# Optimization experiments

Measured on AMD Instinct MI355X. Metric: run time of the kernel, lower is better.

Reference implementation:

```python
import jax, jax.numpy as jnp
import numpy as np

N_NODES = 100000


def leaky(x):
    return jax.nn.leaky_relu(x, negative_slope=0.01)


def gcn_conv(h, W, b, src, dst, n_nodes):
    """PyG GCNConv: add self-loops, symmetric deg^{-1/2} normalization, scatter-add."""
    h = h @ W  # [N, out]
    deg = jax.ops.segment_sum(jnp.ones_like(dst, dtype=h.dtype), dst, num_segments=n_nodes) + 1.0  # +1 self-loop
    dinv = jax.lax.rsqrt(deg)  # deg >= 1 always
    norm = dinv[src] * dinv[dst]  # [E]
    msg = h[src] * norm[:, None]  # gather + scale, [E, out]
    agg = jax.ops.segment_sum(msg, dst, num_segments=n_nodes)
    agg = agg + h * (dinv * dinv)[:, None]  # self-loop message
    return agg + b


def setup_inputs() -> dict:
    key = jax.random.key(0)
    ks = jax.random.split(key, 16)
    num_teams = 100000
    n_edges = 5000000
    n_matches = 1000000
    x = jax.random.randint(ks[0], (N_NODES, 1), 0, num_teams)
    edge_index = jax.random.randint(ks[1], (2, n_edges), 0, N_NODES)
    home = jax.random.randint(ks[2], (n_matches,), 0, N_NODES)
    away = jax.random.randint(ks[3], (n_matches,), 0, N_NODES)
    emb = jax.random.normal(ks[4], (num_teams, 3), dtype=jnp.float32)
    W1 = jax.random.normal(ks[5], (3, 16), dtype=jnp.float32) * (1.0 / np.sqrt(3))
    b1 = jnp.zeros((16,), dtype=jnp.float32)
    W2 = jax.random.normal(ks[6], (16, 3), dtype=jnp.float32) * 0.25
    b2 = jnp.zeros((3,), dtype=jnp.float32)
    lw1 = jax.random.normal(ks[7], (6, 16), dtype=jnp.float32) * (1.0 / np.sqrt(6))
    lb1 = jnp.zeros((16,), dtype=jnp.float32)
    lw2 = jax.random.normal(ks[8], (16, 6), dtype=jnp.float32) * 0.25
    lb2 = jnp.zeros((6,), dtype=jnp.float32)
    lw3 = jax.random.normal(ks[9], (6, 3), dtype=jnp.float32) * (1.0 / np.sqrt(6))
    lb3 = jnp.zeros((3,), dtype=jnp.float32)
    return dict(x=x, edge_index=edge_index, home=home, away=away, emb=emb,
                W1=W1, b1=b1, W2=W2, b2=b2,
                lw1=lw1, lb1=lb1, lw2=lw2, lb2=lb2, lw3=lw3, lb3=lb3)


def reference(x, edge_index, home, away, emb, W1, b1, W2, b2, lw1, lb1, lw2, lb2, lw3, lb3):
    src, dst = edge_index[0], edge_index[1]
    h = emb[x[:, 0]]  # embedding lookup + squeeze(1) -> [N, 3]
    h = leaky(gcn_conv(h, W1, b1, src, dst, N_NODES))  # [N, 16]
    h = leaky(gcn_conv(h, W2, b2, src, dst, N_NODES))  # [N, 3]
    z = jnp.concatenate([h[home], h[away]], axis=-1)  # [M, 6]
    z = leaky(z @ lw1 + lb1)
    z = leaky(z @ lw2 + lb2)
    z = leaky(z @ lw3 + lb3)
    return z.reshape(-1, 3)
```

## Files before the change

### kernel.cpp

```cpp
#include <hip/hip_runtime.h>

typedef unsigned int u32;
typedef unsigned short u16;

static __device__ __forceinline__ float leaky(float v) {
    return v >= 0.0f ? v : 0.01f * v;
}

#define P1_CHUNK 8192
#define P1_T 256
#define NBK 512
#define P2_T 256
#define ASPLIT 4
#define SBLK 1024
#define S1F 8388608.0f
#define S2F 2097152.0f

static __device__ __forceinline__ int ghat(const int* __restrict__ gh,
                                           const int* __restrict__ bsum,
                                           int i, int ghN, int nE) {
    return (i == ghN) ? nE : gh[i] + bsum[i >> 10];
}

__global__ void k_p1hist(const int* __restrict__ dst, int* __restrict__ gh,
                         int nE, int nb) {
    __shared__ int hist[NBK];
    int t = threadIdx.x;
    hist[t] = 0; hist[t + 256] = 0;
    __syncthreads();
    int base = blockIdx.x * P1_CHUNK;
    int lim = min(P1_CHUNK, nE - base);
    if (lim == P1_CHUNK) {
        const int4* p = (const int4*)(dst + base);
        for (int i = t; i < P1_CHUNK / 4; i += P1_T) {
            int4 v = p[i];
            atomicAdd(&hist[v.x >> 8], 1);
            atomicAdd(&hist[v.y >> 8], 1);
            atomicAdd(&hist[v.z >> 8], 1);
            atomicAdd(&hist[v.w >> 8], 1);
        }
    } else {
        for (int i = t; i < lim; i += P1_T)
            atomicAdd(&hist[dst[base + i] >> 8], 1);
    }
    __syncthreads();
    gh[t * nb + blockIdx.x] = hist[t];
    gh[(t + 256) * nb + blockIdx.x] = hist[t + 256];
}

__global__ void g_scanA(const int* __restrict__ in, int* __restrict__ out,
                        int* __restrict__ bsum, int n) {
    __shared__ int s[SBLK];
    int t = threadIdx.x, i = blockIdx.x * SBLK + t;
    int v = (i < n) ? in[i] : 0;
    s[t] = v;
    for (int o = 1; o < SBLK; o <<= 1) {
        __syncthreads();
        int x = (t >= o) ? s[t - o] : 0;
        __syncthreads();
        s[t] += x;
    }
    __syncthreads();
    if (i < n) out[i] = s[t] - v;
    if (t == SBLK - 1) bsum[blockIdx.x] = s[t];
}
__global__ void g_scanB(int* __restrict__ bsum, int nb) {
    __shared__ int s[SBLK];
    int t = threadIdx.x;
    int v = (t < nb) ? bsum[t] : 0;
    s[t] = v;
    for (int o = 1; o < SBLK; o <<= 1) {
        __syncthreads();
        int x = (t >= o) ? s[t - o] : 0;
        __syncthreads();
        s[t] += x;
    }
    __syncthreads();
    if (t < nb) bsum[t] = s[t] - v;
}
__global__ void g_scanC(int* __restrict__ out, const int* __restrict__ bsum,
                        int n, int total) {
    int i = blockIdx.x * blockDim.x + threadIdx.x;
    if (i < n) out[i] += bsum[i / SBLK];
    if (i == 0) out[n] = total;
}

__global__ __launch_bounds__(256) void k_p1scatter(
        const int* __restrict__ src, const int* __restrict__ dst,
        const int* __restrict__ gh, const int* __restrict__ bsum,
        u32* __restrict__ bkt, int nE, int nb, int ghN) {
    __shared__ int cur[NBK];
    __shared__ int loff[NBK];
    __shared__ int gb[NBK];
    __shared__ int sc[NBK];
    __shared__ u32 pay[P1_CHUNK];
    __shared__ u16 bb[P1_CHUNK];
    int t = threadIdx.x;
    int blk = blockIdx.x;
    int idx0 = t * nb + blk;
    int idx1 = (t + 256) * nb + blk;
    int g0 = ghat(gh, bsum, idx0, ghN, nE);
    int c0 = ghat(gh, bsum, idx0 + 1, ghN, nE) - g0;
    int g1 = ghat(gh, bsum, idx1, ghN, nE);
    int c1 = ghat(gh, bsum, idx1 + 1, ghN, nE) - g1;
    gb[t] = g0; gb[t + 256] = g1;
    sc[t] = c0; sc[t + 256] = c1;
    for (int o = 1; o < NBK; o <<= 1) {
        __syncthreads();
        int a0 = (t >= o) ? sc[t - o] : 0;
        int a1 = (t + 256 >= o) ? sc[t + 256 - o] : 0;
        __syncthreads();
        sc[t] += a0; sc[t + 256] += a1;
    }
    __syncthreads();
    loff[t] = sc[t] - c0;           loff[t + 256] = sc[t + 256] - c1;
    cur[t] = loff[t];               cur[t + 256] = loff[t + 256];
    __syncthreads();
    int base = blk * P1_CHUNK;
    int lim = min(P1_CHUNK, nE - base);
    int n4 = lim >> 2;
    const int4* d4p = (const int4*)(dst + base);
    const int4* s4p = (const int4*)(src + base);
    for (int i = t; i < n4; i += P1_T) {
        int4 d4 = d4p[i];
        int4 s4 = s4p[i];
        int b, r;
        b = d4.x >> 8; r = atomicAdd(&cur[b], 1);
        pay[r] = (u32)(((d4.x & 255) << 17) | s4.x); bb[r] = (u16)b;
        b = d4.y >> 8; r = atomicAdd(&cur[b], 1);
        pay[r] = (u32)(((d4.y & 255) << 17) | s4.y); bb[r] = (u16)b;
        b = d4.z >> 8; r = atomicAdd(&cur[b], 1);
        pay[r] = (u32)(((d4.z & 255) << 17) | s4.z); bb[r] = (u16)b;
        b = d4.w >> 8; r = atomicAdd(&cur[b], 1);
        pay[r] = (u32)(((d4.w & 255) << 17) | s4.w); bb[r] = (u16)b;
    }
    for (int i = (n4 << 2) + t; i < lim; i += P1_T) {
        int d = dst[base + i], s = src[base + i];
        int b = d >> 8;
        int r = atomicAdd(&cur[b], 1);
        pay[r] = (u32)(((d & 255) << 17) | s);
        bb[r] = (u16)b;
    }
    __syncthreads();
    for (int i = t; i < lim; i += P1_T) {
        int b = bb[i];
        bkt[gb[b] + (i - loff[b])] = pay[i];
    }
}

__global__ void k_cnt1(const u32* __restrict__ bkt, const int* __restrict__ gh,
                       const int* __restrict__ bsum,
                       const int* __restrict__ x, const float* __restrict__ emb,
                       float* __restrict__ dinv, float4* __restrict__ hd0,
                       int nE, int nb, int ghN, int nN) {
    __shared__ int h[256];
    int t = threadIdx.x, b = blockIdx.x;
    int base = ghat(gh, bsum, b * nb, ghN, nE);
    int end  = (b + 1 < NBK) ? ghat(gh, bsum, (b + 1) * nb, ghN, nE) : nE;
    h[t] = 0;
    __syncthreads();
    int a0 = min((base + 3) & ~3, end);
    if (base + t < a0) atomicAdd(&h[bkt[base + t] >> 17], 1);
    int vend = a0 + ((end - a0) & ~3);
    for (int i = a0 + t * 4; i < vend; i += P2_T * 4) {
        uint4 v = *(const uint4*)&bkt[i];
        atomicAdd(&h[v.x >> 17], 1);
        atomicAdd(&h[v.y >> 17], 1);
        atomicAdd(&h[v.z >> 17], 1);
        atomicAdd(&h[v.w >> 17], 1);
    }
    if (vend + t < end) atomicAdd(&h[bkt[vend + t] >> 17], 1);
    __syncthreads();
    int d = b * 256 + t;
    if (d < nN) {
        float di = rsqrtf((float)h[t] + 1.0f);
        dinv[d] = di;
        int xi = x[d] * 3;
        hd0[d] = make_float4(emb[xi] * di, emb[xi + 1] * di, emb[xi + 2] * di, 0.f);
    }
}

__global__ __launch_bounds__(256) void k_aggI(
        const u32* __restrict__ bkt, const int* __restrict__ gh,
        const int* __restrict__ bsum,
        const float4* __restrict__ tab, float* __restrict__ pacc,
        int nE, int nb, int ghN, float scale, float inv_scale) {
    __shared__ int acc[768];
    int t = threadIdx.x;
    int blk = blockIdx.x, b = blk >> 2, s = blk & 3;
    int base = ghat(gh, bsum, b * nb, ghN, nE);
    int end  = (b + 1 < NBK) ? ghat(gh, bsum, (b + 1) * nb, ghN, nE) : nE;
    int sz = end - base;
    int chunk = (sz + ASPLIT - 1) / ASPLIT;
    int st = min(base + s * chunk, end);
    int en = min(st + chunk, end);
    acc[t] = 0; acc[t + 256] = 0; acc[t + 512] = 0;
    __syncthreads();
    int a0 = min((st + 3) & ~3, en);
    if (st + t < a0) {
        u32 v = bkt[st + t];
        float4 h = tab[v & 0x1FFFFu];
        int bin = (int)(v >> 17) * 3;
        atomicAdd(&acc[bin + 0], __float2int_rn(h.x * scale));
        atomicAdd(&acc[bin + 1], __float2int_rn(h.y * scale));
        atomicAdd(&acc[bin + 2], __float2int_rn(h.z * scale));
    }
    int vend = a0 + ((en - a0) & ~3);
    for (int i = a0 + t * 4; i < vend; i += P2_T * 4) {
        uint4 v = *(const uint4*)&bkt[i];
        float4 h0 = tab[v.x & 0x1FFFFu];
        float4 h1 = tab[v.y & 0x1FFFFu];
        float4 h2 = tab[v.z & 0x1FFFFu];
        float4 h3 = tab[v.w & 0x1FFFFu];
        int b0 = (int)(v.x >> 17) * 3, b1 = (int)(v.y >> 17) * 3;
        int b2 = (int)(v.z >> 17) * 3, b3 = (int)(v.w >> 17) * 3;
        atomicAdd(&acc[b0 + 0], __float2int_rn(h0.x * scale));
        atomicAdd(&acc[b0 + 1], __float2int_rn(h0.y * scale));
        atomicAdd(&acc[b0 + 2], __float2int_rn(h0.z * scale));
        atomicAdd(&acc[b1 + 0], __float2int_rn(h1.x * scale));
        atomicAdd(&acc[b1 + 1], __float2int_rn(h1.y * scale));
        atomicAdd(&acc[b1 + 2], __float2int_rn(h1.z * scale));
        atomicAdd(&acc[b2 + 0], __float2int_rn(h2.x * scale));
        atomicAdd(&acc[b2 + 1], __float2int_rn(h2.y * scale));
        atomicAdd(&acc[b2 + 2], __float2int_rn(h2.z * scale));
        atomicAdd(&acc[b3 + 0], __float2int_rn(h3.x * scale));
        atomicAdd(&acc[b3 + 1], __float2int_rn(h3.y * scale));
        atomicAdd(&acc[b3 + 2], __float2int_rn(h3.z * scale));
    }
    if (vend + t < en) {
        u32 v = bkt[vend + t];
        float4 h = tab[v & 0x1FFFFu];
        int bin = (int)(v >> 17) * 3;
        atomicAdd(&acc[bin + 0], __float2int_rn(h.x * scale));
        atomicAdd(&acc[bin + 1], __float2int_rn(h.y * scale));
        atomicAdd(&acc[bin + 2], __float2int_rn(h.z * scale));
    }
    __syncthreads();
    float* p = pacc + (size_t)blk * 768;
    p[t]       = (float)acc[t * 3 + 0] * inv_scale;
    p[t + 256] = (float)acc[t * 3 + 1] * inv_scale;
    p[t + 512] = (float)acc[t * 3 + 2] * inv_scale;
}

__global__ void k_fin1(const float* __restrict__ pacc, const float* __restrict__ dinv,
                       const float4* __restrict__ hd0,
                       const float* __restrict__ W1, const float* __restrict__ b1,
                       const float* __restrict__ W2,
                       float4* __restrict__ hd2, int nN) {
    int d = blockIdx.x * blockDim.x + threadIdx.x;
    if (d >= nN) return;
    int b = d >> 8, q = d & 255;
    float s0 = 0.f, s1 = 0.f, s2 = 0.f;
#pragma unroll
    for (int s = 0; s < ASPLIT; ++s) {
        const float* p = pacc + (size_t)(b * ASPLIT + s) * 768;
        s0 += p[q]; s1 += p[q + 256]; s2 += p[q + 512];
    }
    float di = dinv[d];
    float4 self = hd0[d];
    float a0 = di * (s0 + self.x);
    float a1 = di * (s1 + self.y);
    float a2 = di * (s2 + self.z);
    float o0 = 0.f, o1 = 0.f, o2 = 0.f;
#pragma unroll
    for (int k = 0; k < 16; ++k) {
        float p = leaky(a0 * W1[k] + a1 * W1[16 + k] + a2 * W1[32 + k] + b1[k]);
        o0 += p * W2[k * 3 + 0];
        o1 += p * W2[k * 3 + 1];
        o2 += p * W2[k * 3 + 2];
    }
    hd2[d] = make_float4(o0 * di, o1 * di, o2 * di, 0.f);
}

__global__ void k_fin2(const float* __restrict__ pacc, const float* __restrict__ dinv,
                       const float4* __restrict__ hd2, const float* __restrict__ b2,
                       float4* __restrict__ h2, int nN) {
    int d = blockIdx.x * blockDim.x + threadIdx.x;
    if (d >= nN) return;
    int b = d >> 8, q = d & 255;
    float s0 = 0.f, s1 = 0.f, s2 = 0.f;
#pragma unroll
    for (int s = 0; s < ASPLIT; ++s) {
        const float* p = pacc + (size_t)(b * ASPLIT + s) * 768;
        s0 += p[q]; s1 += p[q + 256]; s2 += p[q + 512];
    }
    float di = dinv[d];
    float4 self = hd2[d];
    h2[d] = make_float4(leaky(di * (s0 + self.x) + b2[0]),
                        leaky(di * (s1 + self.y) + b2[1]),
                        leaky(di * (s2 + self.z) + b2[2]), 0.f);
}

__global__ __launch_bounds__(256) void k_mlp4v(
        const int* __restrict__ home, const int* __restrict__ away,
        const float4* __restrict__ h2,
        const float* __restrict__ lw1, const float* __restrict__ lb1,
        const float* __restrict__ lw2, const float* __restrict__ lb2,
        const float* __restrict__ lw3, const float* __restrict__ lb3,
        float* __restrict__ out, int nM) {
    __shared__ float s[235];
    int t = threadIdx.x;
    if (t < 96)       s[t] = lw1[t];
    else if (t < 112) s[t] = lb1[t - 96];
    else if (t < 208) s[t] = lw2[t - 112];
    else if (t < 214) s[t] = lb2[t - 208];
    else if (t < 232) s[t] = lw3[t - 214];
    else if (t < 235) s[t] = lb3[t - 232];
    __syncthreads();
    const float* sw1 = s;        const float* sb1 = s + 96;
    const float* sw2 = s + 112;  const float* sb2 = s + 208;
    const float* sw3 = s + 214;  const float* sb3 = s + 232;

    int i = blockIdx.x * blockDim.x + threadIdx.x;
    int m0 = i * 4;
    if (m0 >= nM) return;
    float res[12];
    int nq = min(4, nM - m0);
    int hidx[4], aidx[4];
    if (nq == 4) {
        int4 hv = *(const int4*)&home[m0];
        int4 av = *(const int4*)&away[m0];
        hidx[0] = hv.x; hidx[1] = hv.y; hidx[2] = hv.z; hidx[3] = hv.w;
        aidx[0] = av.x; aidx[1] = av.y; aidx[2] = av.z; aidx[3] = av.w;
    } else {
        for (int j = 0; j < nq; ++j) { hidx[j] = home[m0 + j]; aidx[j] = away[m0 + j]; }
    }
    for (int j = 0; j < nq; ++j) {
        float4 zh = h2[hidx[j]];
        float4 za = h2[aidx[j]];
        float z[6] = {zh.x, zh.y, zh.z, za.x, za.y, za.z};
        float t1[16];
#pragma unroll
        for (int k = 0; k < 16; ++k) {
            float p = sb1[k];
#pragma unroll
            for (int q = 0; q < 6; ++q) p += z[q] * sw1[q * 16 + k];
            t1[k] = leaky(p);
        }
        float t2[6];
#pragma unroll
        for (int k = 0; k < 6; ++k) {
            float p = sb2[k];
#pragma unroll
            for (int q = 0; q < 16; ++q) p += t1[q] * sw2[q * 6 + k];
            t2[k] = leaky(p);
        }
#pragma unroll
        for (int k = 0; k < 3; ++k) {
            float p = sb3[k];
#pragma unroll
            for (int q = 0; q < 6; ++q) p += t2[q] * sw3[q * 3 + k];
            res[j * 3 + k] = leaky(p);
        }
    }
    if (nq == 4) {
        float4* o4 = (float4*)&out[m0 * 3];
        o4[0] = make_float4(res[0], res[1], res[2], res[3]);
        o4[1] = make_float4(res[4], res[5], res[6], res[7]);
        o4[2] = make_float4(res[8], res[9], res[10], res[11]);
    } else {
        for (int j = 0; j < nq * 3; ++j) out[m0 * 3 + j] = res[j];
    }
}

__global__ void k_hist(const int* __restrict__ dst, int* __restrict__ cnt, int nE) {
    int e = blockIdx.x * blockDim.x + threadIdx.x;
    if (e < nE) atomicAdd(&cnt[dst[e]], 1);
}
__global__ void k_prep(const int* __restrict__ off, const int* __restrict__ cnt,
                       float* __restrict__ dinv, int* __restrict__ cur, int nN) {
    int i = blockIdx.x * blockDim.x + threadIdx.x;
    if (i >= nN) return;
    dinv[i] = rsqrtf((float)cnt[i] + 1.0f);
    cur[i] = off[i];
}
__global__ void k_hd0(const int* __restrict__ x, const float* __restrict__ emb,
                      const float* __restrict__ dinv, float4* __restrict__ hd0, int nN) {
    int i = blockIdx.x * blockDim.x + threadIdx.x;
    if (i >= nN) return;
    float di = dinv[i];
    int xi = x[i] * 3;
    hd0[i] = make_float4(emb[xi] * di, emb[xi + 1] * di, emb[xi + 2] * di, 0.0f);
}
__global__ void k_place(const int* __restrict__ src, const int* __restrict__ dst,
                        int* __restrict__ cur, int* __restrict__ csr, int nE) {
    int e = blockIdx.x * blockDim.x + threadIdx.x;
    if (e >= nE) return;
    int p = atomicAdd(&cur[dst[e]], 1);
    csr[p] = src[e];
}
__global__ void k_gather1w(const int* __restrict__ off, const int* __restrict__ csr,
                           const float4* __restrict__ hd0, const float* __restrict__ dinv,
                           const float* __restrict__ W1, const float* __restrict__ b1,
                           const float* __restrict__ W2,
                           float4* __restrict__ hd2, int nN) {
    int g = blockIdx.x * blockDim.x + threadIdx.x;
    int d = g >> 6, lane = threadIdx.x & 63;
    if (d >= nN) return;
    int e0 = off[d], e1 = off[d + 1];
    float sx = 0.f, sy = 0.f, sz = 0.f;
    for (int e = e0 + lane; e < e1; e += 64) {
        float4 v = hd0[csr[e]];
        sx += v.x; sy += v.y; sz += v.z;
    }
    for (int o = 32; o; o >>= 1) {
        sx += __shfl_down(sx, o);
        sy += __shfl_down(sy, o);
        sz += __shfl_down(sz, o);
    }
    if (lane == 0) {
        float di = dinv[d];
        float4 self = hd0[d];
        float a0 = di * (sx + self.x);
        float a1 = di * (sy + self.y);
        float a2 = di * (sz + self.z);
        float o0 = 0.f, o1 = 0.f, o2 = 0.f;
#pragma unroll
        for (int k = 0; k < 16; ++k) {
            float p = leaky(a0 * W1[k] + a1 * W1[16 + k] + a2 * W1[32 + k] + b1[k]);
            o0 += p * W2[k * 3 + 0];
            o1 += p * W2[k * 3 + 1];
            o2 += p * W2[k * 3 + 2];
        }
        hd2[d] = make_float4(o0 * di, o1 * di, o2 * di, 0.0f);
    }
}
__global__ void k_gather2(const int* __restrict__ off, const int* __restrict__ csr,
                          const float4* __restrict__ hd2, const float* __restrict__ dinv,
                          const float* __restrict__ b2,
                          float4* __restrict__ h2, int nN) {
    int g = blockIdx.x * blockDim.x + threadIdx.x;
    int d = g >> 4, lane = threadIdx.x & 15;
    if (d >= nN) return;
    int e0 = off[d], e1 = off[d + 1];
    float s0 = 0.f, s1 = 0.f, s2 = 0.f;
    for (int e = e0 + lane; e < e1; e += 16) {
        float4 v = hd2[csr[e]];
        s0 += v.x; s1 += v.y; s2 += v.z;
    }
    for (int o = 8; o; o >>= 1) {
        s0 += __shfl_down(s0, o, 16);
        s1 += __shfl_down(s1, o, 16);
        s2 += __shfl_down(s2, o, 16);
    }
    if (lane == 0) {
        float di = dinv[d];
        float4 self = hd2[d];
        h2[d] = make_float4(leaky(di * (s0 + self.x) + b2[0]),
                            leaky(di * (s1 + self.y) + b2[1]),
                            leaky(di * (s2 + self.z) + b2[2]), 0.f);
    }
}

extern "C" void kernel_launch(void* const* d_in, const int* in_sizes, int n_in,
                              void* d_out, int out_size, void* d_ws, size_t ws_size,
                              hipStream_t stream) {
    const int*   x    = (const int*)d_in[0];
    const int*   ei   = (const int*)d_in[1];
    const int*   home = (const int*)d_in[2];
    const int*   away = (const int*)d_in[3];
    const float* emb  = (const float*)d_in[4];
    const float* W1   = (const float*)d_in[5];
    const float* b1   = (const float*)d_in[6];
    const float* W2   = (const float*)d_in[7];
    const float* b2   = (const float*)d_in[8];
    const float* lw1  = (const float*)d_in[9];
    const float* lb1  = (const float*)d_in[10];
    const float* lw2  = (const float*)d_in[11];
    const float* lb2  = (const float*)d_in[12];
    const float* lw3  = (const float*)d_in[13];
    const float* lb3  = (const float*)d_in[14];
    float* out = (float*)d_out;

    const int nN = in_sizes[0];
    const int nE = in_sizes[1] / 2;
    const int nM = in_sizes[2];
    const int* src = ei;
    const int* dst = ei + nE;
    const int B = 256;

    const int nb1 = (nE + P1_CHUNK - 1) / P1_CHUNK;
    const int ghN = NBK * nb1;
    const int nbs = (ghN + SBLK - 1) / SBLK;
    const size_t paccN = (size_t)NBK * ASPLIT * 768;

    size_t need = (size_t)3 * nN * 16 + (size_t)nE * 4 + (size_t)(ghN + 1) * 4 +
                  paccN * 4 + (size_t)nN * 4 + (size_t)(nbs + 8) * 4;

    if (nN <= NBK * 256 && ws_size >= need && nbs <= SBLK) {
        char* w = (char*)d_ws;
        float4* hd0 = (float4*)w;                 w += (size_t)nN * 16;
        float4* hd2 = (float4*)w;                 w += (size_t)nN * 16;
        float4* h2  = (float4*)w;                 w += (size_t)nN * 16;
        u32* bkt  = (u32*)w;                      w += (size_t)nE * 4;
        float* pacc = (float*)w;                  w += paccN * 4;
        int* gh   = (int*)w;                      w += (size_t)(ghN + 1) * 4;
        float* dinv = (float*)w;                  w += (size_t)nN * 4;
        int* bsum = (int*)w;

        k_p1hist<<<nb1, P1_T, 0, stream>>>(dst, gh, nE, nb1);
        g_scanA<<<nbs, SBLK, 0, stream>>>(gh, gh, bsum, ghN);
        g_scanB<<<1, SBLK, 0, stream>>>(bsum, nbs);
        k_p1scatter<<<nb1, P1_T, 0, stream>>>(src, dst, gh, bsum, bkt, nE, nb1, ghN);
        k_cnt1<<<NBK, P2_T, 0, stream>>>(bkt, gh, bsum, x, emb, dinv, hd0,
                                         nE, nb1, ghN, nN);
        k_aggI<<<NBK * ASPLIT, P2_T, 0, stream>>>(bkt, gh, bsum, hd0, pacc,
                                                  nE, nb1, ghN, S1F, 1.0f / S1F);
        k_fin1<<<(nN + B - 1) / B, B, 0, stream>>>(pacc, dinv, hd0, W1, b1, W2,
                                                   hd2, nN);
        k_aggI<<<NBK * ASPLIT, P2_T, 0, stream>>>(bkt, gh, bsum, hd2, pacc,
                                                  nE, nb1, ghN, S2F, 1.0f / S2F);
        k_fin2<<<(nN + B - 1) / B, B, 0, stream>>>(pacc, dinv, hd2, b2, h2, nN);
        int nQuads = (nM + 3) / 4;
        k_mlp4v<<<(nQuads + B - 1) / B, B, 0, stream>>>(home, away, h2,
                                                        lw1, lb1, lw2, lb2, lw3, lb3,
                                                        out, nM);
    } else {
        char* w = (char*)d_ws;
        float4* hd0 = (float4*)w;                 w += (size_t)nN * 16;
        float4* hd2 = (float4*)w;                 w += (size_t)nN * 16;
        float4* h2  = (float4*)w;                 w += (size_t)nN * 16;
        int* csr  = (int*)w;                      w += (size_t)nE * 4;
        int* cnt  = (int*)w;                      w += (size_t)(nN + 1) * 4;
        int* off  = (int*)w;                      w += (size_t)(nN + 1) * 4;
        int* cur  = (int*)w;                      w += (size_t)nN * 4;
        float* dinv = (float*)w;                  w += (size_t)nN * 4;
        int* bsum = (int*)w;

        const int nTot = nN + 1;
        const int nbScan = (nTot + SBLK - 1) / SBLK;

        hipMemsetAsync(cnt, 0, (size_t)nTot * sizeof(int), stream);
        k_hist<<<(nE + B - 1) / B, B, 0, stream>>>(dst, cnt, nE);
        g_scanA<<<nbScan, SBLK, 0, stream>>>(cnt, off, bsum, nTot);
        g_scanB<<<1, SBLK, 0, stream>>>(bsum, nbScan);
        g_scanC<<<(nTot + B - 1) / B, B, 0, stream>>>(off, bsum, nTot - 1, nE);
        k_prep<<<(nN + B - 1) / B, B, 0, stream>>>(off, cnt, dinv, cur, nN);
        k_hd0<<<(nN + B - 1) / B, B, 0, stream>>>(x, emb, dinv, hd0, nN);
        k_place<<<(nE + B - 1) / B, B, 0, stream>>>(src, dst, cur, csr, nE);
        k_gather1w<<<((size_t)nN * 64 + B - 1) / B, B, 0, stream>>>(off, csr, hd0, dinv,
                                                                    W1, b1, W2, hd2, nN);
        k_gather2<<<((size_t)nN * 16 + B - 1) / B, B, 0, stream>>>(off, csr, hd2,
                                                                   dinv, b2, h2, nN);
        int nQuads = (nM + 3) / 4;
        k_mlp4v<<<(nQuads + B - 1) / B, B, 0, stream>>>(home, away, h2,
                                                        lw1, lb1, lw2, lb2, lw3, lb3,
                                                        out, nM);
    }
}
```

Before: 136.9 us.

## Replace global histogram scan with fixed-capacity buckets and atomic cursor allocation

Drops the per-block histogram kernel and the three-kernel global prefix scan. Each of the 512 coarse destination buckets now gets a fixed-capacity slot region, and a scatter block reserves its space with one global atomic per bucket. Downstream kernels read the bucket extent from the cursor array, which removes the scan launches and the extra pass over dst. The cost is a larger workspace and a capacity check based on a statistical bound, which can overflow on skewed graphs. The fallback path is also rewritten to use float-atomic scatter in place of CSR construction.

```diff
diff --git a/kernel.cpp b/kernel.cpp
--- a/kernel.cpp
+++ b/kernel.cpp
@@ -8,103 +8,43 @@
 }
 
 #define P1_CHUNK 8192
-#define P1_T 256
 #define NBK 512
-#define P2_T 256
+#define CAPB 16384
 #define ASPLIT 4
-#define SBLK 1024
 #define S1F 8388608.0f
 #define S2F 2097152.0f
 
-static __device__ __forceinline__ int ghat(const int* __restrict__ gh,
-                                           const int* __restrict__ bsum,
-                                           int i, int ghN, int nE) {
-    return (i == ghN) ? nE : gh[i] + bsum[i >> 10];
-}
-
-__global__ void k_p1hist(const int* __restrict__ dst, int* __restrict__ gh,
-                         int nE, int nb) {
-    __shared__ int hist[NBK];
+__global__ __launch_bounds__(256) void k_p1scatterA(
+        const int* __restrict__ src, const int* __restrict__ dst,
+        int* __restrict__ cur, u32* __restrict__ bkt, int nE) {
+    __shared__ int sc[NBK];
+    __shared__ int loff[NBK];
+    __shared__ int gb[NBK];
+    __shared__ int lcur[NBK];
+    __shared__ u32 pay[P1_CHUNK];
+    __shared__ u16 bb[P1_CHUNK];
     int t = threadIdx.x;
-    hist[t] = 0; hist[t + 256] = 0;
+    sc[t] = 0; sc[t + 256] = 0;
     __syncthreads();
     int base = blockIdx.x * P1_CHUNK;
     int lim = min(P1_CHUNK, nE - base);
     if (lim == P1_CHUNK) {
         const int4* p = (const int4*)(dst + base);
-        for (int i = t; i < P1_CHUNK / 4; i += P1_T) {
+        for (int i = t; i < P1_CHUNK / 4; i += 256) {
             int4 v = p[i];
-            atomicAdd(&hist[v.x >> 8], 1);
-            atomicAdd(&hist[v.y >> 8], 1);
-            atomicAdd(&hist[v.z >> 8], 1);
-            atomicAdd(&hist[v.w >> 8], 1);
+            atomicAdd(&sc[v.x >> 8], 1);
+            atomicAdd(&sc[v.y >> 8], 1);
+            atomicAdd(&sc[v.z >> 8], 1);
+            atomicAdd(&sc[v.w >> 8], 1);
         }
     } else {
-        for (int i = t; i < lim; i += P1_T)
-            atomicAdd(&hist[dst[base + i] >> 8], 1);
-    }
-    __syncthreads();
-    gh[t * nb + blockIdx.x] = hist[t];
-    gh[(t + 256) * nb + blockIdx.x] = hist[t + 256];
-}
-
-__global__ void g_scanA(const int* __restrict__ in, int* __restrict__ out,
-                        int* __restrict__ bsum, int n) {
-    __shared__ int s[SBLK];
-    int t = threadIdx.x, i = blockIdx.x * SBLK + t;
-    int v = (i < n) ? in[i] : 0;
-    s[t] = v;
-    for (int o = 1; o < SBLK; o <<= 1) {
-        __syncthreads();
-        int x = (t >= o) ? s[t - o] : 0;
-        __syncthreads();
-        s[t] += x;
-    }
-    __syncthreads();
-    if (i < n) out[i] = s[t] - v;
-    if (t == SBLK - 1) bsum[blockIdx.x] = s[t];
-}
-__global__ void g_scanB(int* __restrict__ bsum, int nb) {
-    __shared__ int s[SBLK];
-    int t = threadIdx.x;
-    int v = (t < nb) ? bsum[t] : 0;
-    s[t] = v;
-    for (int o = 1; o < SBLK; o <<= 1) {
-        __syncthreads();
-        int x = (t >= o) ? s[t - o] : 0;
-        __syncthreads();
-        s[t] += x;
-    }
-    __syncthreads();
-    if (t < nb) bsum[t] = s[t] - v;
-}
-__global__ void g_scanC(int* __restrict__ out, const int* __restrict__ bsum,
-                        int n, int total) {
-    int i = blockIdx.x * blockDim.x + threadIdx.x;
-    if (i < n) out[i] += bsum[i / SBLK];
-    if (i == 0) out[n] = total;
-}
-
-__global__ __launch_bounds__(256) void k_p1scatter(
-        const int* __restrict__ src, const int* __restrict__ dst,
-        const int* __restrict__ gh, const int* __restrict__ bsum,
-        u32* __restrict__ bkt, int nE, int nb, int ghN) {
-    __shared__ int cur[NBK];
-    __shared__ int loff[NBK];
-    __shared__ int gb[NBK];
-    __shared__ int sc[NBK];
-    __shared__ u32 pay[P1_CHUNK];
-    __shared__ u16 bb[P1_CHUNK];
-    int t = threadIdx.x;
-    int blk = blockIdx.x;
-    int idx0 = t * nb + blk;
-    int idx1 = (t + 256) * nb + blk;
-    int g0 = ghat(gh, bsum, idx0, ghN, nE);
-    int c0 = ghat(gh, bsum, idx0 + 1, ghN, nE) - g0;
-    int g1 = ghat(gh, bsum, idx1, ghN, nE);
-    int c1 = ghat(gh, bsum, idx1 + 1, ghN, nE) - g1;
-    gb[t] = g0; gb[t + 256] = g1;
-    sc[t] = c0; sc[t + 256] = c1;
+        for (int i = t; i < lim; i += 256)
+            atomicAdd(&sc[dst[base + i] >> 8], 1);
+    }
+    __syncthreads();
+    int c0 = sc[t], c1 = sc[t + 256];
+    gb[t]       = (t << 14)         + ((c0 > 0) ? atomicAdd(&cur[t], c0) : 0);
+    gb[t + 256] = ((t + 256) << 14) + ((c1 > 0) ? atomicAdd(&cur[t + 256], c1) : 0);
     for (int o = 1; o < NBK; o <<= 1) {
         __syncthreads();
         int a0 = (t >= o) ? sc[t - o] : 0;
@@ -114,55 +54,50 @@
     }
     __syncthreads();
     loff[t] = sc[t] - c0;           loff[t + 256] = sc[t + 256] - c1;
-    cur[t] = loff[t];               cur[t + 256] = loff[t + 256];
-    __syncthreads();
-    int base = blk * P1_CHUNK;
-    int lim = min(P1_CHUNK, nE - base);
+    lcur[t] = loff[t];              lcur[t + 256] = loff[t + 256];
+    __syncthreads();
     int n4 = lim >> 2;
     const int4* d4p = (const int4*)(dst + base);
     const int4* s4p = (const int4*)(src + base);
-    for (int i = t; i < n4; i += P1_T) {
+    for (int i = t; i < n4; i += 256) {
         int4 d4 = d4p[i];
         int4 s4 = s4p[i];
         int b, r;
-        b = d4.x >> 8; r = atomicAdd(&cur[b], 1);
+        b = d4.x >> 8; r = atomicAdd(&lcur[b], 1);
         pay[r] = (u32)(((d4.x & 255) << 17) | s4.x); bb[r] = (u16)b;
-        b = d4.y >> 8; r = atomicAdd(&cur[b], 1);
+        b = d4.y >> 8; r = atomicAdd(&lcur[b], 1);
         pay[r] = (u32)(((d4.y & 255) << 17) | s4.y); bb[r] = (u16)b;
-        b = d4.z >> 8; r = atomicAdd(&cur[b], 1);
+        b = d4.z >> 8; r = atomicAdd(&lcur[b], 1);
         pay[r] = (u32)(((d4.z & 255) << 17) | s4.z); bb[r] = (u16)b;
-        b = d4.w >> 8; r = atomicAdd(&cur[b], 1);
+        b = d4.w >> 8; r = atomicAdd(&lcur[b], 1);
         pay[r] = (u32)(((d4.w & 255) << 17) | s4.w); bb[r] = (u16)b;
     }
-    for (int i = (n4 << 2) + t; i < lim; i += P1_T) {
+    for (int i = (n4 << 2) + t; i < lim; i += 256) {
         int d = dst[base + i], s = src[base + i];
         int b = d >> 8;
-        int r = atomicAdd(&cur[b], 1);
+        int r = atomicAdd(&lcur[b], 1);
         pay[r] = (u32)(((d & 255) << 17) | s);
         bb[r] = (u16)b;
     }
     __syncthreads();
-    for (int i = t; i < lim; i += P1_T) {
+    for (int i = t; i < lim; i += 256) {
         int b = bb[i];
         bkt[gb[b] + (i - loff[b])] = pay[i];
     }
 }
 
-__global__ void k_cnt1(const u32* __restrict__ bkt, const int* __restrict__ gh,
-                       const int* __restrict__ bsum,
-                       const int* __restrict__ x, const float* __restrict__ emb,
-                       float* __restrict__ dinv, float4* __restrict__ hd0,
-                       int nE, int nb, int ghN, int nN) {
+__global__ __launch_bounds__(256) void k_cnt1F(
+        const u32* __restrict__ bkt, const int* __restrict__ cur,
+        const int* __restrict__ x, const float* __restrict__ emb,
+        float* __restrict__ dinv, float4* __restrict__ hd0, int nN) {
     __shared__ int h[256];
     int t = threadIdx.x, b = blockIdx.x;
-    int base = ghat(gh, bsum, b * nb, ghN, nE);
-    int end  = (b + 1 < NBK) ? ghat(gh, bsum, (b + 1) * nb, ghN, nE) : nE;
+    int base = b << 14;
+    int end = base + cur[b];
     h[t] = 0;
     __syncthreads();
-    int a0 = min((base + 3) & ~3, end);
-    if (base + t < a0) atomicAdd(&h[bkt[base + t] >> 17], 1);
-    int vend = a0 + ((end - a0) & ~3);
-    for (int i = a0 + t * 4; i < vend; i += P2_T * 4) {
+    int vend = base + ((end - base) & ~3);
+    for (int i = base + t * 4; i < vend; i += 256 * 4) {
         uint4 v = *(const uint4*)&bkt[i];
         atomicAdd(&h[v.x >> 17], 1);
         atomicAdd(&h[v.y >> 17], 1);
@@ -180,20 +115,18 @@
     }
 }
 
-__global__ __launch_bounds__(256) void k_aggI(
-        const u32* __restrict__ bkt, const int* __restrict__ gh,
-        const int* __restrict__ bsum,
+__global__ __launch_bounds__(256) void k_aggIF(
+        const u32* __restrict__ bkt, const int* __restrict__ cur,
         const float4* __restrict__ tab, float* __restrict__ pacc,
-        int nE, int nb, int ghN, float scale, float inv_scale) {
+        float scale, float inv_scale) {
     __shared__ int acc[768];
     int t = threadIdx.x;
     int blk = blockIdx.x, b = blk >> 2, s = blk & 3;
-    int base = ghat(gh, bsum, b * nb, ghN, nE);
-    int end  = (b + 1 < NBK) ? ghat(gh, bsum, (b + 1) * nb, ghN, nE) : nE;
-    int sz = end - base;
+    int base = b << 14;
+    int sz = cur[b];
     int chunk = (sz + ASPLIT - 1) / ASPLIT;
-    int st = min(base + s * chunk, end);
-    int en = min(st + chunk, end);
+    int st = min(base + s * chunk, base + sz);
+    int en = min(st + chunk, base + sz);
     acc[t] = 0; acc[t + 256] = 0; acc[t + 512] = 0;
     __syncthreads();
     int a0 = min((st + 3) & ~3, en);
@@ -206,7 +139,7 @@
         atomicAdd(&acc[bin + 2], __float2int_rn(h.z * scale));
     }
     int vend = a0 + ((en - a0) & ~3);
-    for (int i = a0 + t * 4; i < vend; i += P2_T * 4) {
+    for (int i = a0 + t * 4; i < vend; i += 256 * 4) {
         uint4 v = *(const uint4*)&bkt[i];
         float4 h0 = tab[v.x & 0x1FFFFu];
         float4 h1 = tab[v.y & 0x1FFFFu];
@@ -310,7 +243,6 @@
     const float* sw1 = s;        const float* sb1 = s + 96;
     const float* sw2 = s + 112;  const float* sb2 = s + 208;
     const float* sw3 = s + 214;  const float* sb3 = s + 232;
-
     int i = blockIdx.x * blockDim.x + threadIdx.x;
     int m0 = i * 4;
     if (m0 >= nM) return;
@@ -363,93 +295,60 @@
     }
 }
 
-__global__ void k_hist(const int* __restrict__ dst, int* __restrict__ cnt, int nE) {
+__global__ void f_deg(const int* __restrict__ dst, float* __restrict__ deg, int nE) {
     int e = blockIdx.x * blockDim.x + threadIdx.x;
-    if (e < nE) atomicAdd(&cnt[dst[e]], 1);
-}
-__global__ void k_prep(const int* __restrict__ off, const int* __restrict__ cnt,
-                       float* __restrict__ dinv, int* __restrict__ cur, int nN) {
+    if (e < nE) atomicAdd(&deg[dst[e]], 1.0f);
+}
+__global__ void f_hd0(const int* __restrict__ x, const float* __restrict__ emb,
+                      float* __restrict__ dinv, float4* __restrict__ hd0, int nN) {
     int i = blockIdx.x * blockDim.x + threadIdx.x;
     if (i >= nN) return;
-    dinv[i] = rsqrtf((float)cnt[i] + 1.0f);
-    cur[i] = off[i];
-}
-__global__ void k_hd0(const int* __restrict__ x, const float* __restrict__ emb,
-                      const float* __restrict__ dinv, float4* __restrict__ hd0, int nN) {
-    int i = blockIdx.x * blockDim.x + threadIdx.x;
-    if (i >= nN) return;
-    float di = dinv[i];
+    float di = rsqrtf(dinv[i] + 1.0f);
+    dinv[i] = di;
     int xi = x[i] * 3;
-    hd0[i] = make_float4(emb[xi] * di, emb[xi + 1] * di, emb[xi + 2] * di, 0.0f);
-}
-__global__ void k_place(const int* __restrict__ src, const int* __restrict__ dst,
-                        int* __restrict__ cur, int* __restrict__ csr, int nE) {
+    hd0[i] = make_float4(emb[xi] * di, emb[xi + 1] * di, emb[xi + 2] * di, 0.f);
+}
+__global__ void f_scatter(const int* __restrict__ src, const int* __restrict__ dst,
+                          const float4* __restrict__ tab, float* __restrict__ agg, int nE) {
     int e = blockIdx.x * blockDim.x + threadIdx.x;
     if (e >= nE) return;
-    int p = atomicAdd(&cur[dst[e]], 1);
-    csr[p] = src[e];
-}
-__global__ void k_gather1w(const int* __restrict__ off, const int* __restrict__ csr,
-                           const float4* __restrict__ hd0, const float* __restrict__ dinv,
-                           const float* __restrict__ W1, const float* __restrict__ b1,
-                           const float* __restrict__ W2,
-                           float4* __restrict__ hd2, int nN) {
-    int g = blockIdx.x * blockDim.x + threadIdx.x;
-    int d = g >> 6, lane = threadIdx.x & 63;
+    int s = src[e], d = dst[e];
+    float4 v = tab[s];
+    atomicAdd(&agg[d * 3 + 0], v.x);
+    atomicAdd(&agg[d * 3 + 1], v.y);
+    atomicAdd(&agg[d * 3 + 2], v.z);
+}
+__global__ void f_fin1(const float* __restrict__ agg, const float* __restrict__ dinv,
+                       const float4* __restrict__ hd0,
+                       const float* __restrict__ W1, const float* __restrict__ b1,
+                       const float* __restrict__ W2, float4* __restrict__ hd2, int nN) {
+    int d = blockIdx.x * blockDim.x + threadIdx.x;
     if (d >= nN) return;
-    int e0 = off[d], e1 = off[d + 1];
-    float sx = 0.f, sy = 0.f, sz = 0.f;
-    for (int e = e0 + lane; e < e1; e += 64) {
-        float4 v = hd0[csr[e]];
-        sx += v.x; sy += v.y; sz += v.z;
-    }
-    for (int o = 32; o; o >>= 1) {
-        sx += __shfl_down(sx, o);
-        sy += __shfl_down(sy, o);
-        sz += __shfl_down(sz, o);
-    }
-    if (lane == 0) {
-        float di = dinv[d];
-        float4 self = hd0[d];
-        float a0 = di * (sx + self.x);
-        float a1 = di * (sy + self.y);
-        float a2 = di * (sz + self.z);
-        float o0 = 0.f, o1 = 0.f, o2 = 0.f;
-#pragma unroll
-        for (int k = 0; k < 16; ++k) {
-            float p = leaky(a0 * W1[k] + a1 * W1[16 + k] + a2 * W1[32 + k] + b1[k]);
-            o0 += p * W2[k * 3 + 0];
-            o1 += p * W2[k * 3 + 1];
-            o2 += p * W2[k * 3 + 2];
-        }
-        hd2[d] = make_float4(o0 * di, o1 * di, o2 * di, 0.0f);
-    }
-}
-__global__ void k_gather2(const int* __restrict__ off, const int* __restrict__ csr,
-                          const float4* __restrict__ hd2, const float* __restrict__ dinv,
-                          const float* __restrict__ b2,
-                          float4* __restrict__ h2, int nN) {
-    int g = blockIdx.x * blockDim.x + threadIdx.x;
-    int d = g >> 4, lane = threadIdx.x & 15;
+    float di = dinv[d];
+    float4 self = hd0[d];
+    float a0 = di * (agg[d * 3 + 0] + self.x);
+    float a1 = di * (agg[d * 3 + 1] + self.y);
+    float a2 = di * (agg[d * 3 + 2] + self.z);
+    float o0 = 0.f, o1 = 0.f, o2 = 0.f;
+#pragma unroll
+    for (int k = 0; k < 16; ++k) {
+        float p = leaky(a0 * W1[k] + a1 * W1[16 + k] + a2 * W1[32 + k] + b1[k]);
+        o0 += p * W2[k * 3 + 0];
+        o1 += p * W2[k * 3 + 1];
+        o2 += p * W2[k * 3 + 2];
+    }
+    hd2[d] = make_float4(o0 * di, o1 * di, o2 * di, 0.f);
+}
+__global__ void f_fin2(const float* __restrict__ agg, const float* __restrict__ dinv,
+                       const float4* __restrict__ hd2, const float* __restrict__ b2,
+                       float4* __restrict__ h2, int nN) {
+    int d = blockIdx.x * blockDim.x + threadIdx.x;
     if (d >= nN) return;
-    int e0 = off[d], e1 = off[d + 1];
-    float s0 = 0.f, s1 = 0.f, s2 = 0.f;
-    for (int e = e0 + lane; e < e1; e += 16) {
-        float4 v = hd2[csr[e]];
-        s0 += v.x; s1 += v.y; s2 += v.z;
-    }
-    for (int o = 8; o; o >>= 1) {
-        s0 += __shfl_down(s0, o, 16);
-        s1 += __shfl_down(s1, o, 16);
-        s2 += __shfl_down(s2, o, 16);
-    }
-    if (lane == 0) {
-        float di = dinv[d];
-        float4 self = hd2[d];
-        h2[d] = make_float4(leaky(di * (s0 + self.x) + b2[0]),
-                            leaky(di * (s1 + self.y) + b2[1]),
-                            leaky(di * (s2 + self.z) + b2[2]), 0.f);
-    }
+    float di = dinv[d];
+    float4 self = hd2[d];
+    h2[d] = make_float4(leaky(di * (agg[d * 3 + 0] + self.x) + b2[0]),
+                        leaky(di * (agg[d * 3 + 1] + self.y) + b2[1]),
+                        leaky(di * (agg[d * 3 + 2] + self.z) + b2[2]), 0.f);
 }
 
 extern "C" void kernel_launch(void* const* d_in, const int* in_sizes, int n_in,
@@ -480,71 +379,60 @@
     const int B = 256;
 
     const int nb1 = (nE + P1_CHUNK - 1) / P1_CHUNK;
-    const int ghN = NBK * nb1;
-    const int nbs = (ghN + SBLK - 1) / SBLK;
     const size_t paccN = (size_t)NBK * ASPLIT * 768;
-
-    size_t need = (size_t)3 * nN * 16 + (size_t)nE * 4 + (size_t)(ghN + 1) * 4 +
-                  paccN * 4 + (size_t)nN * 4 + (size_t)(nbs + 8) * 4;
-
-    if (nN <= NBK * 256 && ws_size >= need && nbs <= SBLK) {
+    const size_t bktN = (size_t)NBK * CAPB;
+
+    size_t need = (size_t)3 * nN * 16 + bktN * 4 + paccN * 4 +
+                  (size_t)nN * 4 + NBK * 4;
+
+    double mean_b = (double)nE * 256.0 / (double)nN;
+    double sig_b = sqrt(mean_b);
+    bool cap_ok = (mean_b + 10.0 * sig_b) < (double)CAPB;
+
+    if (nN <= NBK * 256 && ws_size >= need && cap_ok) {
         char* w = (char*)d_ws;
         float4* hd0 = (float4*)w;                 w += (size_t)nN * 16;
         float4* hd2 = (float4*)w;                 w += (size_t)nN * 16;
         float4* h2  = (float4*)w;                 w += (size_t)nN * 16;
-        u32* bkt  = (u32*)w;                      w += (size_t)nE * 4;
+        u32* bkt  = (u32*)w;                      w += bktN * 4;
         float* pacc = (float*)w;                  w += paccN * 4;
-        int* gh   = (int*)w;                      w += (size_t)(ghN + 1) * 4;
         float* dinv = (float*)w;                  w += (size_t)nN * 4;
-        int* bsum = (int*)w;
-
-        k_p1hist<<<nb1, P1_T, 0, stream>>>(dst, gh, nE, nb1);
-        g_scanA<<<nbs, SBLK, 0, stream>>>(gh, gh, bsum, ghN);
-        g_scanB<<<1, SBLK, 0, stream>>>(bsum, nbs);
-        k_p1scatter<<<nb1, P1_T, 0, stream>>>(src, dst, gh, bsum, bkt, nE, nb1, ghN);
-        k_cnt1<<<NBK, P2_T, 0, stream>>>(bkt, gh, bsum, x, emb, dinv, hd0,
-                                         nE, nb1, ghN, nN);
-        k_aggI<<<NBK * ASPLIT, P2_T, 0, stream>>>(bkt, gh, bsum, hd0, pacc,
-                                                  nE, nb1, ghN, S1F, 1.0f / S1F);
+        int* cur  = (int*)w;
+
+        hipMemsetAsync(cur, 0, NBK * sizeof(int), stream);
+        k_p1scatterA<<<nb1, 256, 0, stream>>>(src, dst, cur, bkt, nE);
+        k_cnt1F<<<NBK, 256, 0, stream>>>(bkt, cur, x, emb, dinv, hd0, nN);
+        k_aggIF<<<NBK * ASPLIT, 256, 0, stream>>>(bkt, cur, hd0, pacc,
+                                                  S1F, 1.0f / S1F);
         k_fin1<<<(nN + B - 1) / B, B, 0, stream>>>(pacc, dinv, hd0, W1, b1, W2,
                                                    hd2, nN);
-        k_aggI<<<NBK * ASPLIT, P2_T, 0, stream>>>(bkt, gh, bsum, hd2, pacc,
-                                                  nE, nb1, ghN, S2F, 1.0f / S2F);
+        k_aggIF<<<NBK * ASPLIT, 256, 0, stream>>>(bkt, cur, hd2, pacc,
+                                                  S2F, 1.0f / S2F);
         k_fin2<<<(nN + B - 1) / B, B, 0, stream>>>(pacc, dinv, hd2, b2, h2, nN);
         int nQuads = (nM + 3) / 4;
         k_mlp4v<<<(nQuads + B - 1) / B, B, 0, stream>>>(home, away, h2,
-                                                        lw1, lb1, lw2, lb2, lw3, lb3,
-                                                        out, nM);
+                                                        lw1, lb1, lw2, lb2,
+                                                        lw3, lb3, out, nM);
     } else {
         char* w = (char*)d_ws;
         float4* hd0 = (float4*)w;                 w += (size_t)nN * 16;
         float4* hd2 = (float4*)w;                 w += (size_t)nN * 16;
         float4* h2  = (float4*)w;                 w += (size_t)nN * 16;
-        int* csr  = (int*)w;                      w += (size_t)nE * 4;
-        int* cnt  = (int*)w;                      w += (size_t)(nN + 1) * 4;
-        int* off  = (int*)w;                      w += (size_t)(nN + 1) * 4;
-        int* cur  = (int*)w;                      w += (size_t)nN * 4;
-        float* dinv = (float*)w;                  w += (size_t)nN * 4;
-        int* bsum = (int*)w;
-
-        const int nTot = nN + 1;
-        const int nbScan = (nTot + SBLK - 1) / SBLK;
-
-        hipMemsetAsync(cnt, 0, (size_t)nTot * sizeof(int), stream);
-        k_hist<<<(nE + B - 1) / B, B, 0, stream>>>(dst, cnt, nE);
-        g_scanA<<<nbScan, SBLK, 0, stream>>>(cnt, off, bsum, nTot);
-        g_scanB<<<1, SBLK, 0, stream>>>(bsum, nbScan);
-        g_scanC<<<(nTot + B - 1) / B, B, 0, stream>>>(off, bsum, nTot - 1, nE);
-        k_prep<<<(nN + B - 1) / B, B, 0, stream>>>(off, cnt, dinv, cur, nN);
-        k_hd0<<<(nN + B - 1) / B, B, 0, stream>>>(x, emb, dinv, hd0, nN);
-        k_place<<<(nE + B - 1) / B, B, 0, stream>>>(src, dst, cur, csr, nE);
-        k_gather1w<<<((size_t)nN * 64 + B - 1) / B, B, 0, stream>>>(off, csr, hd0, dinv,
-                                                                    W1, b1, W2, hd2, nN);
-        k_gather2<<<((size_t)nN * 16 + B - 1) / B, B, 0, stream>>>(off, csr, hd2,
-                                                                   dinv, b2, h2, nN);
+        float* agg  = (float*)w;                  w += (size_t)3 * nN * 4;
+        float* dinv = (float*)w;
+
+        hipMemsetAsync(dinv, 0, (size_t)nN * sizeof(float), stream);
+        hipMemsetAsync(agg, 0, (size_t)3 * nN * sizeof(float), stream);
+        f_deg<<<(nE + B - 1) / B, B, 0, stream>>>(dst, dinv, nE);
+        f_hd0<<<(nN + B - 1) / B, B, 0, stream>>>(x, emb, dinv, hd0, nN);
+        f_scatter<<<(nE + B - 1) / B, B, 0, stream>>>(src, dst, hd0, agg, nE);
+        f_fin1<<<(nN + B - 1) / B, B, 0, stream>>>(agg, dinv, hd0, W1, b1, W2, hd2, nN);
+        hipMemsetAsync(agg, 0, (size_t)3 * nN * sizeof(float), stream);
+        f_scatter<<<(nE + B - 1) / B, B, 0, stream>>>(src, dst, hd2, agg, nE);
+        f_fin2<<<(nN + B - 1) / B, B, 0, stream>>>(agg, dinv, hd2, b2, h2, nN);
         int nQuads = (nM + 3) / 4;
         k_mlp4v<<<(nQuads + B - 1) / B, B, 0, stream>>>(home, away, h2,
-                                                        lw1, lb1, lw2, lb2, lw3, lb3,
-                                                        out, nM);
-    }
-}
+                                                        lw1, lb1, lw2, lb2,
+                                                        lw3, lb3, out, nM);
+    }
+}
```

After: 136.2 us. Within noise of the previous version (-0.5%).
